# Performance work log

Measured on AMD Instinct MI355X. Metric: run time of the kernel, lower is better.

Reference implementation:

```python
import jax, jax.numpy as jnp
import numpy as np

VOC, D, CPR, RELS = 2048, 128, 128, 7
B, DEPTH = 512, 4  # complete binary trees: 2**DEPTH leaves per tree


def setup_inputs() -> dict:
    key = jax.random.key(0)
    ks = jax.random.split(key, 13)
    s = lambda k, shape, fan: jax.random.normal(k, shape, jnp.float32) / np.sqrt(fan)
    return {
        "leaf_ids": jax.random.randint(ks[0], (B, 2, 2 ** DEPTH), 0, VOC),
        "Wv": s(ks[1], (D, VOC), VOC), "bv": jnp.zeros((D,), jnp.float32),
        "Wcps": s(ks[2], (D, 2 * D), 2 * D), "bcps": jnp.zeros((D,), jnp.float32),
        "Wcpst": s(ks[3], (D, D * D), D * D), "bcpst": jnp.zeros((D,), jnp.float32),
        "Wcpr": s(ks[4], (CPR, 2 * D), 2 * D), "bcpr": jnp.zeros((CPR,), jnp.float32),
        "Wcprt": s(ks[5], (CPR, D * D), D * D), "bcprt": jnp.zeros((CPR,), jnp.float32),
        "Wsm": s(ks[6], (RELS, CPR), CPR), "bsm": jnp.zeros((RELS,), jnp.float32),
    }


def reference(leaf_ids, Wv, bv, Wcps, bcps, Wcpst, bcpst, Wcpr, bcpr, Wcprt, bcprt, Wsm, bsm):
    d = Wv.shape[0]
    # leaf embedding: voc(one_hot(idx)) == Wv[:, idx] + bv  -> [B, 2, L, d]
    h = jnp.take(Wv.T, leaf_ids, axis=0) + bv
    # batched level-by-level tree composition (complete binary trees)
    while h.shape[2] > 1:
        l, r = h[:, :, 0::2, :], h[:, :, 1::2, :]
        lin = jnp.concatenate([l, r], axis=-1) @ Wcps.T + bcps
        kron = (l[..., :, None] * r[..., None, :]).reshape(l.shape[:-1] + (d * d,))
        h = jnp.tanh(lin + kron @ Wcpst.T + bcpst)
    lc, rc = h[:, 0, 0, :], h[:, 1, 0, :]  # [B, d] each
    cpr = jnp.concatenate([lc, rc], axis=-1) @ Wcpr.T + bcpr
    kron = (lc[:, :, None] * rc[:, None, :]).reshape(lc.shape[0], d * d)
    act = jax.nn.leaky_relu(cpr + kron @ Wcprt.T + bcprt, 0.01)
    logits = act @ Wsm.T + bsm
    return jax.nn.log_softmax(logits, axis=-1)  # [B, RELS]
```

## Files before the change

### kernel.cpp

```cpp
#include <hip/hip_runtime.h>
#include <hip/hip_bf16.h>
#include <hip/hip_fp16.h>

#define DD    128
#define VOCAB 2048
#define NRELS 7
#define NWF   (130 * 16384)

typedef _Float16 f16;
typedef __attribute__((ext_vector_type(8))) _Float16 f16x8;
typedef __attribute__((ext_vector_type(4))) float    f32x4;

__device__ __forceinline__ float lde(const void* p, size_t i, int bf) {
    if (bf) return (float)((const __hip_bfloat16*)p)[i];
    return ((const float*)p)[i];
}

__device__ __forceinline__ int detect_bf(const unsigned short* wv) {
    int sane = 0;
    #pragma unroll
    for (int i = 0; i < 64; ++i) {
        unsigned e = (wv[i] >> 7) & 0xFFu;
        sane += (e >= 90u && e <= 160u) ? 1 : 0;
    }
    return sane == 64;
}

__global__ void prep_all(const void* Wv, const void* bv,
                         const void* Wcps, const void* bcps,
                         const void* Wcpst, const void* bcpst,
                         const void* Wcpr, const void* bcpr,
                         const void* Wcprt, const void* bcprt,
                         const void* Wsm, const void* bsm,
                         f16* __restrict__ WvT, f16* __restrict__ Wext, f16* __restrict__ Wfin,
                         float* __restrict__ bias_lvl, float* __restrict__ bias_fin,
                         float* __restrict__ Wsm_f, float* __restrict__ bsm_f)
{
    const int bf = detect_bf((const unsigned short*)Wv);
    const int b = blockIdx.x;
    const int tid = threadIdx.x;

    if (b < 64) {
        __shared__ float tile[64][65];
        int vt = b >> 1, dt = b & 1;
        int tx = tid & 63, ty = tid >> 6;
        for (int yy = ty; yy < 64; yy += 4)
            tile[yy][tx] = lde(Wv, (size_t)(dt * 64 + yy) * VOCAB + vt * 64 + tx, bf);
        __syncthreads();
        for (int yy = ty; yy < 64; yy += 4) {
            int v = vt * 64 + yy, d = dt * 64 + tx;
            WvT[(size_t)v * DD + d] = (f16)(tile[tx][yy] + lde(bv, d, bf));
        }
        return;
    }
    if (b >= 2144) {
        if (tid < 128)      bias_lvl[tid] = lde(bcps, tid, bf) + lde(bcpst, tid, bf);
        else if (tid < 256) bias_fin[tid - 128] = lde(bcpr, tid - 128, bf) + lde(bcprt, tid - 128, bf);
        for (int o = tid; o < NRELS * DD; o += 256) Wsm_f[o] = lde(Wsm, o, bf);
        if (tid < NRELS) bsm_f[tid] = lde(bsm, tid, bf);
        return;
    }
    const int bb    = b - 64;
    const int which = bb / 1040;
    const int rem   = bb - which * 1040;
    const int i     = rem >> 3;
    const int n8    = rem & 7;
    const void* Wt = which ? (const void*)Wcprt : (const void*)Wcpst;
    const void* Ws = which ? (const void*)Wcpr  : (const void*)Wcps;
    f16* dst = which ? Wfin : Wext;

    __shared__ float tile[16 * 129];
    #pragma unroll
    for (int it = 0; it < 8; ++it) {
        int idx = it * 256 + tid;
        int rr = idx >> 7, c = idx & 127;
        float v = (i < 128) ? lde(Wt, (size_t)(n8 * 16 + rr) * 16384 + (size_t)i * 128 + c, bf)
                            : lde(Ws, (size_t)(n8 * 16 + rr) * 256 + (size_t)(i - 128) * 128 + c, bf);
        tile[rr * 129 + c] = v;
    }
    __syncthreads();
    f16* out = dst + (size_t)(i * 8 + n8) * 2048;
    #pragma unroll
    for (int it = 0; it < 8; ++it) {
        int o = it * 256 + tid;
        int t = o >> 9, ln = (o >> 3) & 63, e = o & 7;
        out[o] = (f16)tile[(ln & 15) * 129 + t * 32 + ((ln >> 4) << 3) + e];
    }
}

__launch_bounds__(128, 2)
__global__ void gemm_kernel(const f16* __restrict__ hin, const int* __restrict__ ids,
                            const f16* __restrict__ Wf,
                            f16* __restrict__ part, int Mrows, int S, int BI)
{
    __shared__ f16 Lt[128 * 128];

    const int tid  = threadIdx.x;
    const int lane = tid & 63;
    const int wv   = tid >> 6;
    const int b    = blockIdx.x;
    const int nh   = (b >> 2) & 1;
    const int r    = ((b >> 3) << 2) | (b & 3);
    const int mb   = r / S;
    const int s    = r - mb * S;
    const int m0   = mb * 128;
    const int i0   = s * BI;
    const int nI   = BI + ((s == 1 || s == 2) ? 1 : 0);

    #pragma unroll
    for (int it = 0; it < 16; ++it) {
        int c  = it * 128 + tid;
        int mm = c >> 4;
        int cb = c & 15;
        int row = ids ? ids[2 * (m0 + mm)] : 2 * (m0 + mm);
        f16x8 v = *(const f16x8*)&hin[(size_t)row * DD + cb * 8];
        *(f16x8*)&Lt[mm * 128 + ((cb ^ (mm & 15)) << 3)] = v;
    }

    const int mrow = lane & 15;
    const int q    = lane >> 4;
    const int wm   = wv * 64;

    f16x8 rf[4][4];
    #pragma unroll
    for (int mt = 0; mt < 4; ++mt) {
        int p = m0 + wm + mt * 16 + mrow;
        int row = ids ? ids[2 * p + 1] : 2 * p + 1;
        #pragma unroll
        for (int t = 0; t < 4; ++t)
            rf[mt][t] = *(const f16x8*)&hin[(size_t)row * DD + t * 32 + q * 8];
    }

    __syncthreads();

    auto imap = [&](int ii) { return (ii < BI) ? (i0 + ii) : (s == 1 ? 128 : 129); };
    const f16* wb0 = Wf + nh * 8192 + lane * 8;
    auto ldW = [&](int ic, int tt, f16x8* d) {
        const f16* p = wb0 + (size_t)imap(ic) * 16384 + tt * 512;
        #pragma unroll
        for (int nt = 0; nt < 4; ++nt) d[nt] = *(const f16x8*)(p + nt * 2048);
    };
    auto lpRead = [&](int i, int mt) -> f16 {
        return Lt[(wm + mt * 16 + mrow) * 128 + (((i >> 3) ^ mrow) << 3) + (i & 7)];
    };

    f32x4 acc[4][4] = {};
    f16x8 wbuf[2][4];
    f16 lpv[4], lpn[4];

    ldW(0, 0, wbuf[0]);
    ldW(0, 1, wbuf[1]);
    {
        int i = imap(0);
        if (i < 128) {
            #pragma unroll
            for (int mt = 0; mt < 4; ++mt) lpv[mt] = lpRead(i, mt);
        }
    }

#define TSTEP(T) {                                                                      \
    const f16x8* wc = wbuf[(T) & 1];                                                    \
    if (i < 128) {                                                                      \
        _Pragma("unroll")                                                               \
        for (int mt = 0; mt < 4; ++mt) {                                                \
            f16x8 a = lb[mt] * rf[mt][T];                                               \
            _Pragma("unroll")                                                           \
            for (int nt = 0; nt < 4; ++nt)                                              \
                acc[mt][nt] = __builtin_amdgcn_mfma_f32_16x16x32_f16(a, wc[nt], acc[mt][nt], 0, 0, 0); \
        }                                                                               \
    } else if (i == 128) {                                                              \
        _Pragma("unroll")                                                               \
        for (int mt = 0; mt < 4; ++mt) {                                                \
            f16x8 a = *(const f16x8*)&Lt[(wm + mt * 16 + mrow) * 128 + ((((T) * 4 + q) ^ mrow) << 3)]; \
            _Pragma("unroll")                                                           \
            for (int nt = 0; nt < 4; ++nt)                                              \
                acc[mt][nt] = __builtin_amdgcn_mfma_f32_16x16x32_f16(a, wc[nt], acc[mt][nt], 0, 0, 0); \
        }                                                                               \
    } else {                                                                            \
        _Pragma("unroll")                                                               \
        for (int mt = 0; mt < 4; ++mt) {                                                \
            _Pragma("unroll")                                                           \
            for (int nt = 0; nt < 4; ++nt)                                              \
                acc[mt][nt] = __builtin_amdgcn_mfma_f32_16x16x32_f16(rf[mt][T], wc[nt], acc[mt][nt], 0, 0, 0); \
        }                                                                               \
    } }

    for (int ii = 0; ii < nI; ++ii) {
        const int i = imap(ii);
        const bool more = (ii + 1 < nI);
        f16x8 lb[4];
        if (i < 128) {
            #pragma unroll
            for (int mt = 0; mt < 4; ++mt) {
                f16 v = lpv[mt];
                #pragma unroll
                for (int e = 0; e < 8; ++e) lb[mt][e] = v;
            }
        }
        TSTEP(0);
        ldW(ii, 2, wbuf[0]);
        TSTEP(1);
        ldW(ii, 3, wbuf[1]);
        if (more) {
            int i2 = imap(ii + 1);
            if (i2 < 128) {
                #pragma unroll
                for (int mt = 0; mt < 4; ++mt) lpn[mt] = lpRead(i2, mt);
            }
        }
        TSTEP(2);
        if (more) ldW(ii + 1, 0, wbuf[0]);
        TSTEP(3);
        if (more) ldW(ii + 1, 1, wbuf[1]);
        #pragma unroll
        for (int mt = 0; mt < 4; ++mt) lpv[mt] = lpn[mt];
    }
#undef TSTEP

    f16* pb = part + ((size_t)s * Mrows + m0) * DD + nh * 64;
    #pragma unroll
    for (int mt = 0; mt < 4; ++mt)
        #pragma unroll
        for (int nt = 0; nt < 4; ++nt) {
            int colg = nt * 16 + mrow;
            #pragma unroll
            for (int rr = 0; rr < 4; ++rr) {
                int rowl = wm + mt * 16 + q * 4 + rr;
                pb[(size_t)rowl * DD + colg] = (f16)acc[mt][nt][rr];
            }
        }
}

__global__ void epi_level(const f16* __restrict__ part, const float* __restrict__ bias,
                          f16* __restrict__ hout, int Mrows, int S)
{
    int idx = (blockIdx.x * 256 + threadIdx.x) * 8;
    size_t stride = (size_t)Mrows * DD;
    float sum[8] = {};
    for (int s2 = 0; s2 < S; ++s2) {
        f16x8 v = *(const f16x8*)&part[(size_t)s2 * stride + idx];
        #pragma unroll
        for (int e = 0; e < 8; ++e) sum[e] += (float)v[e];
    }
    int n = idx & 127;
    f16x8 o;
    #pragma unroll
    for (int e = 0; e < 8; ++e) o[e] = (f16)tanhf(sum[e] + bias[n + e]);
    *(f16x8*)&hout[idx] = o;
}

__global__ void fin_epi(const f16* __restrict__ part, const float* __restrict__ bias,
                        const float* __restrict__ Wsm_f, const float* __restrict__ bsm_f,
                        const unsigned short* __restrict__ wv_raw, void* __restrict__ outp, int S)
{
    int lane = threadIdx.x & 63;
    int wv = threadIdx.x >> 6;
    int p = blockIdx.x * 4 + wv;
    size_t stride = (size_t)512 * DD;
    const f16* base = part + (size_t)p * DD;
    float a0 = 0.f, a1 = 0.f;
    for (int s2 = 0; s2 < S; ++s2) {
        a0 += (float)base[(size_t)s2 * stride + lane];
        a1 += (float)base[(size_t)s2 * stride + 64 + lane];
    }
    a0 += bias[lane];      a1 += bias[64 + lane];
    a0 = (a0 > 0.f) ? a0 : 0.01f * a0;
    a1 = (a1 > 0.f) ? a1 : 0.01f * a1;
    float lg[NRELS];
    #pragma unroll
    for (int r = 0; r < NRELS; ++r) {
        float pr = a0 * Wsm_f[r * DD + lane] + a1 * Wsm_f[r * DD + 64 + lane];
        #pragma unroll
        for (int d = 1; d < 64; d <<= 1) pr += __shfl_xor(pr, d, 64);
        lg[r] = pr + bsm_f[r];
    }
    float mx = lg[0];
    #pragma unroll
    for (int r = 1; r < NRELS; ++r) mx = fmaxf(mx, lg[r]);
    float se = 0.f;
    #pragma unroll
    for (int r = 0; r < NRELS; ++r) se += expf(lg[r] - mx);
    float lse = logf(se) + mx;
    if (lane < NRELS) {
        float v = lg[lane] - lse;
        if (detect_bf(wv_raw)) ((__hip_bfloat16*)outp)[p * NRELS + lane] = __float2bfloat16(v);
        else                   ((float*)outp)[p * NRELS + lane] = v;
    }
}

extern "C" void kernel_launch(void* const* d_in, const int* in_sizes, int n_in,
                              void* d_out, int out_size, void* d_ws, size_t ws_size,
                              hipStream_t stream)
{
    const int* ids = (const int*)d_in[0];

    char* ws = (char*)d_ws;
    f16*   part     = (f16*)ws;
    f16*   h1       = (f16*)(ws + ((size_t)20 << 20));
    f16*   h2       = (f16*)(ws + ((size_t)22 << 20));
    f16*   h3       = (f16*)(ws + ((size_t)23 << 20));
    f16*   h4       = (f16*)(ws + ((size_t)23 << 20) + (512 << 10));
    f16*   WvT      = (f16*)(ws + ((size_t)24 << 20));
    f16*   Wext     = (f16*)(ws + ((size_t)24 << 20) + (512 << 10));
    f16*   Wfin     = Wext + (size_t)NWF;
    float* bias_lvl = (float*)(Wfin + (size_t)NWF);
    float* bias_fin = bias_lvl + 128;
    float* Wsm_f    = bias_fin + 128;
    float* bsm_f    = Wsm_f + NRELS * DD;

    if (ws_size < ((size_t)34 << 20)) return;

    prep_all<<<2145, 256, 0, stream>>>(d_in[1], d_in[2], d_in[3], d_in[4], d_in[5], d_in[6],
                                       d_in[7], d_in[8], d_in[9], d_in[10], d_in[11], d_in[12],
                                       WvT, Wext, Wfin, bias_lvl, bias_fin, Wsm_f, bsm_f);

    gemm_kernel<<<1024, 128, 0, stream>>>(WvT, ids, Wext, part, 8192, 8, 16);
    epi_level<<<512, 256, 0, stream>>>(part, bias_lvl, h1, 8192, 8);
    gemm_kernel<<<1024, 128, 0, stream>>>(h1, nullptr, Wext, part, 4096, 16, 8);
    epi_level<<<256, 256, 0, stream>>>(part, bias_lvl, h2, 4096, 16);
    gemm_kernel<<<1024, 128, 0, stream>>>(h2, nullptr, Wext, part, 2048, 32, 4);
    epi_level<<<128, 256, 0, stream>>>(part, bias_lvl, h3, 2048, 32);
    gemm_kernel<<<512, 128, 0, stream>>>(h3, nullptr, Wext, part, 1024, 32, 4);
    epi_level<<<64, 256, 0, stream>>>(part, bias_lvl, h4, 1024, 32);
    gemm_kernel<<<512, 128, 0, stream>>>(h4, nullptr, Wfin, part, 512, 64, 2);
    fin_epi<<<128, 256, 0, stream>>>(part, bias_fin, Wsm_f, bsm_f,
                                     (const unsigned short*)d_in[1], d_out, 64);
}
```

Measured before the change: 284.2 us.

## Use 4-wave GEMM blocks with 32-row warp tiles and fewer K-splits

Each GEMM block now runs 4 wavefronts of 32 rows each instead of 2 wavefronts of 64 rows. Per-wave accumulator and register use is halved, and launch bounds are raised to allow 3 blocks per CU. Weight loads are regrouped into two 8-register pair buffers that prefetch the next K-step. Split-K counts are halved on the later levels, so fewer partial sums go through epilogue reduction, at the cost of more K work per block and fewer blocks.

After: 270.3 us. 1.05x faster.

```diff
diff --git a/kernel.cpp b/kernel.cpp
--- a/kernel.cpp
+++ b/kernel.cpp
@@ -88,7 +88,7 @@
     }
 }
 
-__launch_bounds__(128, 2)
+__launch_bounds__(256, 3)
 __global__ void gemm_kernel(const f16* __restrict__ hin, const int* __restrict__ ids,
                             const f16* __restrict__ Wf,
                             f16* __restrict__ part, int Mrows, int S, int BI)
@@ -108,8 +108,8 @@
     const int nI   = BI + ((s == 1 || s == 2) ? 1 : 0);
 
     #pragma unroll
-    for (int it = 0; it < 16; ++it) {
-        int c  = it * 128 + tid;
+    for (int it = 0; it < 8; ++it) {
+        int c  = it * 256 + tid;
         int mm = c >> 4;
         int cb = c & 15;
         int row = ids ? ids[2 * (m0 + mm)] : 2 * (m0 + mm);
@@ -119,11 +119,11 @@
 
     const int mrow = lane & 15;
     const int q    = lane >> 4;
-    const int wm   = wv * 64;
-
-    f16x8 rf[4][4];
-    #pragma unroll
-    for (int mt = 0; mt < 4; ++mt) {
+    const int wm   = wv * 32;
+
+    f16x8 rf[2][4];
+    #pragma unroll
+    for (int mt = 0; mt < 2; ++mt) {
         int p = m0 + wm + mt * 16 + mrow;
         int row = ids ? ids[2 * p + 1] : 2 * p + 1;
         #pragma unroll
@@ -135,91 +135,86 @@
 
     auto imap = [&](int ii) { return (ii < BI) ? (i0 + ii) : (s == 1 ? 128 : 129); };
     const f16* wb0 = Wf + nh * 8192 + lane * 8;
-    auto ldW = [&](int ic, int tt, f16x8* d) {
-        const f16* p = wb0 + (size_t)imap(ic) * 16384 + tt * 512;
-        #pragma unroll
-        for (int nt = 0; nt < 4; ++nt) d[nt] = *(const f16x8*)(p + nt * 2048);
-    };
     auto lpRead = [&](int i, int mt) -> f16 {
         return Lt[(wm + mt * 16 + mrow) * 128 + (((i >> 3) ^ mrow) << 3) + (i & 7)];
     };
 
-    f32x4 acc[4][4] = {};
-    f16x8 wbuf[2][4];
-    f16 lpv[4], lpn[4];
-
-    ldW(0, 0, wbuf[0]);
-    ldW(0, 1, wbuf[1]);
+    f32x4 acc[2][4] = {};
+    f16x8 wA[8], wB[8];
+    f16 lpv[2], lpn[2], lb0[8], lb1[8];
+
+#define LDPAIR(ic, P, ARR) {                                                           \
+    const f16* _p = wb0 + (size_t)imap(ic) * 16384 + (P) * 1024;                       \
+    _Pragma("unroll")                                                                  \
+    for (int u = 0; u < 8; ++u)                                                        \
+        ARR[u] = *(const f16x8*)(_p + ((u >> 2) * 512) + (u & 3) * 2048);              \
+    }
+
+    LDPAIR(0, 0, wA);
+    LDPAIR(0, 1, wB);
     {
         int i = imap(0);
         if (i < 128) {
             #pragma unroll
-            for (int mt = 0; mt < 4; ++mt) lpv[mt] = lpRead(i, mt);
-        }
-    }
-
-#define TSTEP(T) {                                                                      \
-    const f16x8* wc = wbuf[(T) & 1];                                                    \
+            for (int mt = 0; mt < 2; ++mt) lpv[mt] = lpRead(i, mt);
+        }
+    }
+
+#define TSTEP(T, ARR, BASE) {                                                           \
     if (i < 128) {                                                                      \
         _Pragma("unroll")                                                               \
-        for (int mt = 0; mt < 4; ++mt) {                                                \
-            f16x8 a = lb[mt] * rf[mt][T];                                               \
+        for (int mt = 0; mt < 2; ++mt) {                                                \
+            f16x8 a = (mt ? *(f16x8*)lb1 : *(f16x8*)lb0) * rf[mt][T];                   \
             _Pragma("unroll")                                                           \
             for (int nt = 0; nt < 4; ++nt)                                              \
-                acc[mt][nt] = __builtin_amdgcn_mfma_f32_16x16x32_f16(a, wc[nt], acc[mt][nt], 0, 0, 0); \
+                acc[mt][nt] = __builtin_amdgcn_mfma_f32_16x16x32_f16(a, ARR[(BASE)+nt], acc[mt][nt], 0, 0, 0); \
         }                                                                               \
     } else if (i == 128) {                                                              \
         _Pragma("unroll")                                                               \
-        for (int mt = 0; mt < 4; ++mt) {                                                \
+        for (int mt = 0; mt < 2; ++mt) {                                                \
             f16x8 a = *(const f16x8*)&Lt[(wm + mt * 16 + mrow) * 128 + ((((T) * 4 + q) ^ mrow) << 3)]; \
             _Pragma("unroll")                                                           \
             for (int nt = 0; nt < 4; ++nt)                                              \
-                acc[mt][nt] = __builtin_amdgcn_mfma_f32_16x16x32_f16(a, wc[nt], acc[mt][nt], 0, 0, 0); \
+                acc[mt][nt] = __builtin_amdgcn_mfma_f32_16x16x32_f16(a, ARR[(BASE)+nt], acc[mt][nt], 0, 0, 0); \
         }                                                                               \
     } else {                                                                            \
         _Pragma("unroll")                                                               \
-        for (int mt = 0; mt < 4; ++mt) {                                                \
+        for (int mt = 0; mt < 2; ++mt) {                                                \
             _Pragma("unroll")                                                           \
             for (int nt = 0; nt < 4; ++nt)                                              \
-                acc[mt][nt] = __builtin_amdgcn_mfma_f32_16x16x32_f16(rf[mt][T], wc[nt], acc[mt][nt], 0, 0, 0); \
+                acc[mt][nt] = __builtin_amdgcn_mfma_f32_16x16x32_f16(rf[mt][T], ARR[(BASE)+nt], acc[mt][nt], 0, 0, 0); \
         }                                                                               \
     } }
 
     for (int ii = 0; ii < nI; ++ii) {
-        const int i = imap(ii);
-        const bool more = (ii + 1 < nI);
-        f16x8 lb[4];
+        const int i   = imap(ii);
+        const int iin = (ii + 1 < nI) ? (ii + 1) : (nI - 1);
         if (i < 128) {
             #pragma unroll
-            for (int mt = 0; mt < 4; ++mt) {
-                f16 v = lpv[mt];
-                #pragma unroll
-                for (int e = 0; e < 8; ++e) lb[mt][e] = v;
-            }
-        }
-        TSTEP(0);
-        ldW(ii, 2, wbuf[0]);
-        TSTEP(1);
-        ldW(ii, 3, wbuf[1]);
-        if (more) {
-            int i2 = imap(ii + 1);
+            for (int e = 0; e < 8; ++e) { lb0[e] = lpv[0]; lb1[e] = lpv[1]; }
+        }
+        TSTEP(0, wA, 0);
+        TSTEP(1, wA, 4);
+        LDPAIR(iin, 0, wA);
+        {
+            int i2 = imap(iin);
             if (i2 < 128) {
                 #pragma unroll
-                for (int mt = 0; mt < 4; ++mt) lpn[mt] = lpRead(i2, mt);
+                for (int mt = 0; mt < 2; ++mt) lpn[mt] = lpRead(i2, mt);
             }
         }
-        TSTEP(2);
-        if (more) ldW(ii + 1, 0, wbuf[0]);
-        TSTEP(3);
-        if (more) ldW(ii + 1, 1, wbuf[1]);
-        #pragma unroll
-        for (int mt = 0; mt < 4; ++mt) lpv[mt] = lpn[mt];
+        TSTEP(2, wB, 0);
+        TSTEP(3, wB, 4);
+        LDPAIR(iin, 1, wB);
+        #pragma unroll
+        for (int mt = 0; mt < 2; ++mt) lpv[mt] = lpn[mt];
     }
 #undef TSTEP
+#undef LDPAIR
 
     f16* pb = part + ((size_t)s * Mrows + m0) * DD + nh * 64;
     #pragma unroll
-    for (int mt = 0; mt < 4; ++mt)
+    for (int mt = 0; mt < 2; ++mt)
         #pragma unroll
         for (int nt = 0; nt < 4; ++nt) {
             int colg = nt * 16 + mrow;
@@ -314,15 +309,15 @@
                                        d_in[7], d_in[8], d_in[9], d_in[10], d_in[11], d_in[12],
                                        WvT, Wext, Wfin, bias_lvl, bias_fin, Wsm_f, bsm_f);
 
-    gemm_kernel<<<1024, 128, 0, stream>>>(WvT, ids, Wext, part, 8192, 8, 16);
+    gemm_kernel<<<1024, 256, 0, stream>>>(WvT, ids, Wext, part, 8192, 8, 16);
     epi_level<<<512, 256, 0, stream>>>(part, bias_lvl, h1, 8192, 8);
-    gemm_kernel<<<1024, 128, 0, stream>>>(h1, nullptr, Wext, part, 4096, 16, 8);
-    epi_level<<<256, 256, 0, stream>>>(part, bias_lvl, h2, 4096, 16);
-    gemm_kernel<<<1024, 128, 0, stream>>>(h2, nullptr, Wext, part, 2048, 32, 4);
-    epi_level<<<128, 256, 0, stream>>>(part, bias_lvl, h3, 2048, 32);
-    gemm_kernel<<<512, 128, 0, stream>>>(h3, nullptr, Wext, part, 1024, 32, 4);
-    epi_level<<<64, 256, 0, stream>>>(part, bias_lvl, h4, 1024, 32);
-    gemm_kernel<<<512, 128, 0, stream>>>(h4, nullptr, Wfin, part, 512, 64, 2);
+    gemm_kernel<<<512, 256, 0, stream>>>(h1, nullptr, Wext, part, 4096, 8, 16);
+    epi_level<<<256, 256, 0, stream>>>(part, bias_lvl, h2, 4096, 8);
+    gemm_kernel<<<512, 256, 0, stream>>>(h2, nullptr, Wext, part, 2048, 16, 8);
+    epi_level<<<128, 256, 0, stream>>>(part, bias_lvl, h3, 2048, 16);
+    gemm_kernel<<<256, 256, 0, stream>>>(h3, nullptr, Wext, part, 1024, 16, 8);
+    epi_level<<<64, 256, 0, stream>>>(part, bias_lvl, h4, 1024, 16);
+    gemm_kernel<<<256, 256, 0, stream>>>(h4, nullptr, Wfin, part, 512, 32, 4);
     fin_epi<<<128, 256, 0, stream>>>(part, bias_fin, Wsm_f, bsm_f,
-                                     (const unsigned short*)d_in[1], d_out, 64);
-}
+                                     (const unsigned short*)d_in[1], d_out, 32);
+}
```

## Stage weight tiles through LDS with async global_load_lds double buffering

Applied to the files above, without the earlier changes.

The GEMM kernel no longer stages the full 128x128 left-operand tile in LDS. Instead each block loads only the BI left-operand values it needs into registers. Weight slices are streamed through double-buffered LDS with async global_load_lds, and the loop is templated on BI so it fully unrolls. This removes the per-block left-tile staging and the register-held weight prefetch. The cost is a __syncthreads per i-step plus LDS reads for the weights, and the tail path now reloads the left rows from global memory.

Result: faster. 271.5 us (-4.4%).

```diff
diff --git a/kernel.cpp b/kernel.cpp
--- a/kernel.cpp
+++ b/kernel.cpp
@@ -88,12 +88,13 @@
     }
 }
 
+template<int BI>
 __launch_bounds__(128, 2)
 __global__ void gemm_kernel(const f16* __restrict__ hin, const int* __restrict__ ids,
                             const f16* __restrict__ Wf,
-                            f16* __restrict__ part, int Mrows, int S, int BI)
-{
-    __shared__ f16 Lt[128 * 128];
+                            f16* __restrict__ part, int Mrows, int S)
+{
+    __shared__ f16 Wb[2][8192];
 
     const int tid  = threadIdx.x;
     const int lane = tid & 63;
@@ -105,115 +106,96 @@
     const int s    = r - mb * S;
     const int m0   = mb * 128;
     const int i0   = s * BI;
-    const int nI   = BI + ((s == 1 || s == 2) ? 1 : 0);
-
-    #pragma unroll
-    for (int it = 0; it < 16; ++it) {
-        int c  = it * 128 + tid;
-        int mm = c >> 4;
-        int cb = c & 15;
-        int row = ids ? ids[2 * (m0 + mm)] : 2 * (m0 + mm);
-        f16x8 v = *(const f16x8*)&hin[(size_t)row * DD + cb * 8];
-        *(f16x8*)&Lt[mm * 128 + ((cb ^ (mm & 15)) << 3)] = v;
-    }
+    const bool tail = (s == 1 || s == 2);
 
     const int mrow = lane & 15;
     const int q    = lane >> 4;
     const int wm   = wv * 64;
 
     f16x8 rf[4][4];
+    int rowL[4];
     #pragma unroll
     for (int mt = 0; mt < 4; ++mt) {
         int p = m0 + wm + mt * 16 + mrow;
         int row = ids ? ids[2 * p + 1] : 2 * p + 1;
+        rowL[mt] = ids ? ids[2 * p] : 2 * p;
         #pragma unroll
         for (int t = 0; t < 4; ++t)
             rf[mt][t] = *(const f16x8*)&hin[(size_t)row * DD + t * 32 + q * 8];
     }
 
+    f16 lw[4][BI];
+    #pragma unroll
+    for (int mt = 0; mt < 4; ++mt) {
+        const f16* src = &hin[(size_t)rowL[mt] * DD + i0];
+        if constexpr (BI == 16) { *(f16x8*)&lw[mt][0] = *(const f16x8*)src;
+                                  *(f16x8*)&lw[mt][8] = *(const f16x8*)(src + 8); }
+        else if constexpr (BI == 8) { *(f16x8*)&lw[mt][0] = *(const f16x8*)src; }
+        else if constexpr (BI == 4) { *(unsigned long long*)&lw[mt][0] = *(const unsigned long long*)src; }
+        else { *(unsigned int*)&lw[mt][0] = *(const unsigned int*)src; }
+    }
+
+    auto stage = [&](int i, int buf) {
+        const f16* g = Wf + (size_t)i * 16384 + nh * 8192 + (size_t)(wv * 64 + lane) * 8;
+        #pragma unroll
+        for (int k = 0; k < 8; ++k) {
+            const f16* gg = g + k * 1024;
+            f16* l = &Wb[buf][(k * 2 + wv) * 512];
+            __builtin_amdgcn_global_load_lds(
+                (const __attribute__((address_space(1))) unsigned int*)gg,
+                (__attribute__((address_space(3))) unsigned int*)l, 16, 0, 0);
+        }
+    };
+
+    stage(i0, 0);
     __syncthreads();
 
-    auto imap = [&](int ii) { return (ii < BI) ? (i0 + ii) : (s == 1 ? 128 : 129); };
-    const f16* wb0 = Wf + nh * 8192 + lane * 8;
-    auto ldW = [&](int ic, int tt, f16x8* d) {
-        const f16* p = wb0 + (size_t)imap(ic) * 16384 + tt * 512;
-        #pragma unroll
-        for (int nt = 0; nt < 4; ++nt) d[nt] = *(const f16x8*)(p + nt * 2048);
-    };
-    auto lpRead = [&](int i, int mt) -> f16 {
-        return Lt[(wm + mt * 16 + mrow) * 128 + (((i >> 3) ^ mrow) << 3) + (i & 7)];
-    };
-
     f32x4 acc[4][4] = {};
-    f16x8 wbuf[2][4];
-    f16 lpv[4], lpn[4];
-
-    ldW(0, 0, wbuf[0]);
-    ldW(0, 1, wbuf[1]);
-    {
-        int i = imap(0);
-        if (i < 128) {
-            #pragma unroll
-            for (int mt = 0; mt < 4; ++mt) lpv[mt] = lpRead(i, mt);
-        }
-    }
-
-#define TSTEP(T) {                                                                      \
-    const f16x8* wc = wbuf[(T) & 1];                                                    \
-    if (i < 128) {                                                                      \
+
+#define TSTEP(T, BUF, KRON, LBV)                                                        \
+    {                                                                                   \
+        f16x8 wc[4];                                                                    \
+        _Pragma("unroll")                                                               \
+        for (int nt = 0; nt < 4; ++nt)                                                  \
+            wc[nt] = *(const f16x8*)&Wb[BUF][nt * 2048 + (T) * 512 + lane * 8];         \
         _Pragma("unroll")                                                               \
         for (int mt = 0; mt < 4; ++mt) {                                                \
-            f16x8 a = lb[mt] * rf[mt][T];                                               \
+            f16x8 a = (KRON) ? (LBV[mt] * rf[mt][T]) : rf[mt][T];                       \
             _Pragma("unroll")                                                           \
             for (int nt = 0; nt < 4; ++nt)                                              \
                 acc[mt][nt] = __builtin_amdgcn_mfma_f32_16x16x32_f16(a, wc[nt], acc[mt][nt], 0, 0, 0); \
         }                                                                               \
-    } else if (i == 128) {                                                              \
-        _Pragma("unroll")                                                               \
-        for (int mt = 0; mt < 4; ++mt) {                                                \
-            f16x8 a = *(const f16x8*)&Lt[(wm + mt * 16 + mrow) * 128 + ((((T) * 4 + q) ^ mrow) << 3)]; \
-            _Pragma("unroll")                                                           \
-            for (int nt = 0; nt < 4; ++nt)                                              \
-                acc[mt][nt] = __builtin_amdgcn_mfma_f32_16x16x32_f16(a, wc[nt], acc[mt][nt], 0, 0, 0); \
-        }                                                                               \
-    } else {                                                                            \
-        _Pragma("unroll")                                                               \
-        for (int mt = 0; mt < 4; ++mt) {                                                \
-            _Pragma("unroll")                                                           \
-            for (int nt = 0; nt < 4; ++nt)                                              \
-                acc[mt][nt] = __builtin_amdgcn_mfma_f32_16x16x32_f16(rf[mt][T], wc[nt], acc[mt][nt], 0, 0, 0); \
-        }                                                                               \
-    } }
-
-    for (int ii = 0; ii < nI; ++ii) {
-        const int i = imap(ii);
-        const bool more = (ii + 1 < nI);
+    }
+
+    #pragma unroll
+    for (int ii = 0; ii < BI; ++ii) {
+        const int buf = ii & 1;
+        if (ii + 1 < BI)      stage(i0 + ii + 1, buf ^ 1);
+        else if (tail)        stage(s == 1 ? 128 : 129, buf ^ 1);
         f16x8 lb[4];
-        if (i < 128) {
+        #pragma unroll
+        for (int mt = 0; mt < 4; ++mt) {
+            f16 v = lw[mt][ii];
             #pragma unroll
-            for (int mt = 0; mt < 4; ++mt) {
-                f16 v = lpv[mt];
+            for (int e = 0; e < 8; ++e) lb[mt][e] = v;
+        }
+        TSTEP(0, buf, true, lb); TSTEP(1, buf, true, lb);
+        TSTEP(2, buf, true, lb); TSTEP(3, buf, true, lb);
+        __syncthreads();
+    }
+
+    if (tail) {
+        const int buf = BI & 1;
+        if (s == 1) {
+            #pragma unroll
+            for (int mt = 0; mt < 4; ++mt)
                 #pragma unroll
-                for (int e = 0; e < 8; ++e) lb[mt][e] = v;
-            }
-        }
-        TSTEP(0);
-        ldW(ii, 2, wbuf[0]);
-        TSTEP(1);
-        ldW(ii, 3, wbuf[1]);
-        if (more) {
-            int i2 = imap(ii + 1);
-            if (i2 < 128) {
-                #pragma unroll
-                for (int mt = 0; mt < 4; ++mt) lpn[mt] = lpRead(i2, mt);
-            }
-        }
-        TSTEP(2);
-        if (more) ldW(ii + 1, 0, wbuf[0]);
-        TSTEP(3);
-        if (more) ldW(ii + 1, 1, wbuf[1]);
-        #pragma unroll
-        for (int mt = 0; mt < 4; ++mt) lpv[mt] = lpn[mt];
+                for (int t = 0; t < 4; ++t)
+                    rf[mt][t] = *(const f16x8*)&hin[(size_t)rowL[mt] * DD + t * 32 + q * 8];
+        }
+        f16x8 dummy[4];
+        TSTEP(0, buf, false, dummy); TSTEP(1, buf, false, dummy);
+        TSTEP(2, buf, false, dummy); TSTEP(3, buf, false, dummy);
     }
 #undef TSTEP
 
@@ -314,15 +296,15 @@
                                        d_in[7], d_in[8], d_in[9], d_in[10], d_in[11], d_in[12],
                                        WvT, Wext, Wfin, bias_lvl, bias_fin, Wsm_f, bsm_f);
 
-    gemm_kernel<<<1024, 128, 0, stream>>>(WvT, ids, Wext, part, 8192, 8, 16);
+    gemm_kernel<16><<<1024, 128, 0, stream>>>(WvT, ids, Wext, part, 8192, 8);
     epi_level<<<512, 256, 0, stream>>>(part, bias_lvl, h1, 8192, 8);
-    gemm_kernel<<<1024, 128, 0, stream>>>(h1, nullptr, Wext, part, 4096, 16, 8);
+    gemm_kernel<8><<<1024, 128, 0, stream>>>(h1, nullptr, Wext, part, 4096, 16);
     epi_level<<<256, 256, 0, stream>>>(part, bias_lvl, h2, 4096, 16);
-    gemm_kernel<<<1024, 128, 0, stream>>>(h2, nullptr, Wext, part, 2048, 32, 4);
+    gemm_kernel<4><<<1024, 128, 0, stream>>>(h2, nullptr, Wext, part, 2048, 32);
     epi_level<<<128, 256, 0, stream>>>(part, bias_lvl, h3, 2048, 32);
-    gemm_kernel<<<512, 128, 0, stream>>>(h3, nullptr, Wext, part, 1024, 32, 4);
+    gemm_kernel<4><<<512, 128, 0, stream>>>(h3, nullptr, Wext, part, 1024, 32);
     epi_level<<<64, 256, 0, stream>>>(part, bias_lvl, h4, 1024, 32);
-    gemm_kernel<<<512, 128, 0, stream>>>(h4, nullptr, Wfin, part, 512, 64, 2);
+    gemm_kernel<2><<<512, 128, 0, stream>>>(h4, nullptr, Wfin, part, 512, 64);
     fin_epi<<<128, 256, 0, stream>>>(part, bias_fin, Wsm_f, bsm_f,
                                      (const unsigned short*)d_in[1], d_out, 64);
 }
```
